# Kernel optimization log

Measured on AMD Instinct MI355X. Metric: run time of the kernel, lower is better.

## Reference

```python
import jax, jax.numpy as jnp
import numpy as np

DILATIONS = [1, 2, 4, 8, 16, 32, 64, 128, 256, 512] * 2  # 20 layers
C = 128      # residual channels
S = 128      # skip channels
K = 3        # kernel size
B = 8        # batch
T = 8192     # timesteps


def _causal_dilated_conv(x, W, b, dilation):
    # x: [B, Cin, T], W: [Cout, Cin, K] -> [B, Cout, T], left-padded (causal)
    pad = (W.shape[-1] - 1) * dilation
    y = jax.lax.conv_general_dilated(
        x, W, window_strides=(1,), padding=[(pad, 0)],
        rhs_dilation=(dilation,), dimension_numbers=('NCH', 'OIH', 'NCH'))
    return y + b[None, :, None]


def setup_inputs() -> dict:
    key = jax.random.key(0)
    ks = jax.random.split(key, 7)
    L = len(DILATIONS)
    scale = 0.05
    x = jax.random.normal(ks[0], (B, C, T), dtype=jnp.float32)
    # gated activation: dilated conv emits 2*C channels (tanh half + sigmoid half)
    Wconv = jax.random.normal(ks[1], (L, 2 * C, C, K), dtype=jnp.float32) * scale
    bconv = jax.random.normal(ks[2], (L, 2 * C), dtype=jnp.float32) * scale
    Wout = jax.random.normal(ks[3], (L, C, C), dtype=jnp.float32) * scale
    bout = jax.random.normal(ks[4], (L, C), dtype=jnp.float32) * scale
    Wskip = jax.random.normal(ks[5], (L, S, C), dtype=jnp.float32) * scale
    bskip = jax.random.normal(ks[6], (L, S), dtype=jnp.float32) * scale
    return {"x": x, "Wconv": Wconv, "bconv": bconv, "Wout": Wout,
            "bout": bout, "Wskip": Wskip, "bskip": bskip}


def reference(x, Wconv, bconv, Wout, bout, Wskip, bskip):
    L = len(DILATIONS)
    skips = []
    for i, d in enumerate(DILATIONS):
        y = _causal_dilated_conv(x, Wconv[i], bconv[i], d)       # [B, 2C, T]
        a, g = jnp.split(y, 2, axis=1)
        z = jnp.tanh(a) * jax.nn.sigmoid(g)                       # gated, [B, C, T]
        skips.append(jnp.einsum('sc,bct->bst', Wskip[i], z) + bskip[i][None, :, None])
        if i < L - 1:
            out = jnp.einsum('oc,bct->bot', Wout[i], z) + bout[i][None, :, None]
        else:
            out = z  # last layer: use_output_transform = False
        x = out + x  # residual add
    return x, jnp.stack(skips)  # ([B,C,T], [L,B,S,T])
```

## Files before the change

kernel.cpp:

```cpp
#include <hip/hip_runtime.h>
#include <hip/hip_bf16.h>

#define L_NUM 20
#define CC 128
#define TB 8192
#define BB 8
#define TT 64

#define NCONV (L_NUM * 3 * 256 * 128)
#define NMAT  (L_NUM * 128 * 128)
#define XN    ((size_t)BB * TB * CC)

typedef __attribute__((ext_vector_type(4))) float f32x4;
typedef __attribute__((ext_vector_type(8))) short bf16x8;
typedef unsigned int u32;

static const int DILS[L_NUM] = {1, 2, 4, 8, 16, 32, 64, 128, 256, 512,
                                1, 2, 4, 8, 16, 32, 64, 128, 256, 512};

__device__ __forceinline__ unsigned short f2b(float f) {
  union { __hip_bfloat16 h; unsigned short u; } cv;
  cv.h = __float2bfloat16(f);
  return cv.u;
}
__device__ __forceinline__ float b2fu(u32 u) {
  union { u32 u; float f; } cv;
  cv.u = u << 16;
  return cv.f;
}

__device__ __forceinline__ int swz(int t, int cbyte) {
  return (t * 256 + cbyte) ^ ((t & 7) << 4);
}

__device__ __forceinline__ void gload16(const void* g, void* l) {
  __builtin_amdgcn_global_load_lds(
      (const __attribute__((address_space(1))) u32*)g,
      (__attribute__((address_space(3))) u32*)l, 16, 0, 0);
}

__global__ void prep_kernel(const float* __restrict__ Wconv,
                            const float* __restrict__ Wout,
                            const float* __restrict__ Wskip,
                            unsigned short* __restrict__ wc,
                            unsigned short* __restrict__ wo,
                            unsigned short* __restrict__ wsk,
                            unsigned short* __restrict__ zp) {
  int i = blockIdx.x * 256 + threadIdx.x;
  if (i < 128) zp[i] = 0;
  if (i < NCONV) {
    int c = i & 127;
    int o = (i >> 7) & 255;
    int lk = i >> 15;
    int k = lk % 3;
    int l = lk / 3;
    wc[i] = f2b(Wconv[((size_t)(l * 256 + o) * 128 + c) * 3 + k]);
  }
  if (i < NMAT) {
    wo[i]  = f2b(Wout[i]);
    wsk[i] = f2b(Wskip[i]);
  }
}

__global__ __launch_bounds__(256) void x0t_kernel(const float* __restrict__ x0,
                                                  unsigned short* __restrict__ hi,
                                                  unsigned short* __restrict__ lo) {
  __shared__ unsigned short Hs[TT * CC], Ls[TT * CC];
  const int tid = threadIdx.x, lane = tid & 63, w = tid >> 6;
  const int b = blockIdx.y, t0 = blockIdx.x * TT;
  const float* xb = x0 + (size_t)b * CC * TB;
#pragma unroll
  for (int it = 0; it < 8; ++it) {
    int c0 = it * 16 + w * 4;
    u32 hu[4], lu[4];
#pragma unroll
    for (int i2 = 0; i2 < 4; ++i2) {
      float v = xb[(size_t)(c0 + i2) * TB + t0 + lane];
      unsigned short h = f2b(v);
      hu[i2] = h;
      lu[i2] = f2b(v - b2fu(h));
    }
    uint2 hp, lp;
    hp.x = hu[0] | (hu[1] << 16); hp.y = hu[2] | (hu[3] << 16);
    lp.x = lu[0] | (lu[1] << 16); lp.y = lu[2] | (lu[3] << 16);
    *reinterpret_cast<uint2*>(reinterpret_cast<char*>(Hs) + swz(lane, c0 * 2)) = hp;
    *reinterpret_cast<uint2*>(reinterpret_cast<char*>(Ls) + swz(lane, c0 * 2)) = lp;
  }
  __syncthreads();
  unsigned short* hb = hi + ((size_t)b * TB + t0) * CC;
  unsigned short* lb = lo + ((size_t)b * TB + t0) * CC;
#pragma unroll
  for (int it = 0; it < 4; ++it) {
    int o = it * 4096 + tid * 16;
    int t = o >> 8;
    int cl = o & 255;
    int li = t * 256 + (cl ^ ((t & 7) << 4));
    *reinterpret_cast<f32x4*>(reinterpret_cast<char*>(hb) + (size_t)t * 256 + cl) =
        *reinterpret_cast<f32x4*>(reinterpret_cast<char*>(Hs) + li);
    *reinterpret_cast<f32x4*>(reinterpret_cast<char*>(lb) + (size_t)t * 256 + cl) =
        *reinterpret_cast<f32x4*>(reinterpret_cast<char*>(Ls) + li);
  }
}

__global__ __launch_bounds__(512, 4) void layer_kernel(
    const unsigned short* __restrict__ hin,
    unsigned short* __restrict__ hout,
    unsigned short* __restrict__ lob,
    const unsigned short* __restrict__ zpage,
    const unsigned short* __restrict__ Wc,
    const float* __restrict__ bconv,
    const unsigned short* __restrict__ Wo,
    const float* __restrict__ bout,
    const unsigned short* __restrict__ Wsk,
    const float* __restrict__ bskip,
    float* __restrict__ skipo,
    float* __restrict__ fxout,
    int dil, int last) {
  __shared__ unsigned short Xs[3][TT * CC];
  unsigned short* Zs = &Xs[0][0];

  const int tid = threadIdx.x;
  const int lane = tid & 63;
  const int w = tid >> 6;
  const int lo16 = lane & 15;
  const int hi4 = lane >> 4;

  int p = blockIdx.x + (blockIdx.y << 7);
  int xcd = p & 7, ii = p >> 3;
  int bx = (xcd << 4) | (ii >> 3);
  int b = ii & 7;
  int t0 = bx * TT;

  const unsigned short* hb = hin + (size_t)b * TB * CC;

#pragma unroll
  for (int k = 0; k < 3; ++k) {
    int tbase = t0 + (k - 2) * dil;
#pragma unroll
    for (int i = 0; i < 2; ++i) {
      int o = w * 2048 + i * 1024 + lane * 16;
      int tl = o >> 8;
      int cb = (o & 255) ^ ((tl & 7) << 4);
      int tg = tbase + tl;
      const char* src = (tg >= 0)
          ? (reinterpret_cast<const char*>(hb + (size_t)tg * CC) + cb)
          : (reinterpret_cast<const char*>(zpage) + cb);
      gload16(src, reinterpret_cast<char*>(&Xs[k][0]) + w * 2048 + i * 1024);
    }
  }
  __syncthreads();

  f32x4 zero4 = {0.f, 0.f, 0.f, 0.f};
  f32x4 accA[4], accG[4];
#pragma unroll
  for (int j = 0; j < 4; ++j) { accA[j] = zero4; accG[j] = zero4; }

#pragma unroll
  for (int k = 0; k < 3; ++k) {
    const unsigned short* Wk = Wc + k * 256 * 128;
#pragma unroll
    for (int kk = 0; kk < 4; ++kk) {
      int c0 = kk * 32 + hi4 * 8;
      bf16x8 aA = *reinterpret_cast<const bf16x8*>(Wk + (w * 16 + lo16) * 128 + c0);
      bf16x8 aG = *reinterpret_cast<const bf16x8*>(Wk + (128 + w * 16 + lo16) * 128 + c0);
#pragma unroll
      for (int j = 0; j < 4; ++j) {
        bf16x8 bx8 = *reinterpret_cast<const bf16x8*>(
            reinterpret_cast<const char*>(&Xs[k][0]) + swz(j * 16 + lo16, c0 * 2));
        accA[j] = __builtin_amdgcn_mfma_f32_16x16x32_bf16(aA, bx8, accA[j], 0, 0, 0);
        accG[j] = __builtin_amdgcn_mfma_f32_16x16x32_bf16(aG, bx8, accG[j], 0, 0, 0);
      }
    }
  }

  f32x4 bca = *reinterpret_cast<const f32x4*>(bconv + w * 16 + hi4 * 4);
  f32x4 bcg = *reinterpret_cast<const f32x4*>(bconv + 128 + w * 16 + hi4 * 4);
  uint2 zpk[4];
#pragma unroll
  for (int j = 0; j < 4; ++j) {
    u32 zu[4];
#pragma unroll
    for (int reg = 0; reg < 4; ++reg) {
      float a = accA[j][reg] + bca[reg];
      float g = accG[j][reg] + bcg[reg];
      float ea = __builtin_amdgcn_exp2f(2.885390081777927f * a);
      float th = 1.f - 2.f * __builtin_amdgcn_rcpf(1.f + ea);
      float sg = __builtin_amdgcn_rcpf(
          1.f + __builtin_amdgcn_exp2f(-1.4426950408889634f * g));
      zu[reg] = f2b(th * sg);
    }
    zpk[j].x = zu[0] | (zu[1] << 16);
    zpk[j].y = zu[2] | (zu[3] << 16);
  }

  const unsigned short* lb = lob + (size_t)b * TB * CC;
  uint2 hres[4], lres[4];
#pragma unroll
  for (int j = 0; j < 4; ++j) {
    int t = t0 + j * 16 + lo16;
    int cB = w * 16 + hi4 * 4;
    hres[j] = *reinterpret_cast<const uint2*>(hb + (size_t)t * CC + cB);
    lres[j] = *reinterpret_cast<const uint2*>(lb + (size_t)t * CC + cB);
  }
  f32x4 bsk = *reinterpret_cast<const f32x4*>(bskip + w * 16 + hi4 * 4);
  f32x4 bo  = *reinterpret_cast<const f32x4*>(bout + w * 16 + hi4 * 4);

  __syncthreads();

#pragma unroll
  for (int j = 0; j < 4; ++j) {
    int cB = w * 16 + hi4 * 4;
    *reinterpret_cast<uint2*>(reinterpret_cast<char*>(Zs) +
                              swz(j * 16 + lo16, cB * 2)) = zpk[j];
  }
  __syncthreads();

  f32x4 accS[4], accO[4];
#pragma unroll
  for (int j = 0; j < 4; ++j) { accS[j] = zero4; accO[j] = zero4; }

#pragma unroll
  for (int kk = 0; kk < 4; ++kk) {
    int c0 = kk * 32 + hi4 * 8;
    bf16x8 aS = *reinterpret_cast<const bf16x8*>(Wsk + (w * 16 + lo16) * 128 + c0);
    bf16x8 aO = *reinterpret_cast<const bf16x8*>(Wo + (w * 16 + lo16) * 128 + c0);
#pragma unroll
    for (int j = 0; j < 4; ++j) {
      bf16x8 bz = *reinterpret_cast<const bf16x8*>(
          reinterpret_cast<const char*>(Zs) + swz(j * 16 + lo16, c0 * 2));
      accS[j] = __builtin_amdgcn_mfma_f32_16x16x32_bf16(aS, bz, accS[j], 0, 0, 0);
      accO[j] = __builtin_amdgcn_mfma_f32_16x16x32_bf16(aO, bz, accO[j], 0, 0, 0);
    }
  }

  float* skb = skipo + (size_t)b * CC * TB;
  float* fxb = fxout + (size_t)b * CC * TB;
  unsigned short* hrow = hout + (size_t)b * TB * CC;
  unsigned short* lrow = lob + (size_t)b * TB * CC;

#pragma unroll
  for (int j = 0; j < 4; ++j) {
    int t = j * 16 + lo16;
    int cB = w * 16 + hi4 * 4;
    u32 hu[4] = {hres[j].x & 0xffffu, hres[j].x >> 16,
                 hres[j].y & 0xffffu, hres[j].y >> 16};
    u32 lu[4] = {lres[j].x & 0xffffu, lres[j].x >> 16,
                 lres[j].y & 0xffffu, lres[j].y >> 16};
#pragma unroll
    for (int reg = 0; reg < 4; ++reg)
      skb[(size_t)(cB + reg) * TB + t0 + t] = accS[j][reg] + bsk[reg];
    if (last) {
      uint2 zp2 = *reinterpret_cast<const uint2*>(
          reinterpret_cast<const char*>(Zs) + swz(t, cB * 2));
      u32 zu[4] = {zp2.x & 0xffffu, zp2.x >> 16, zp2.y & 0xffffu, zp2.y >> 16};
#pragma unroll
      for (int reg = 0; reg < 4; ++reg)
        fxb[(size_t)(cB + reg) * TB + t0 + t] =
            b2fu(zu[reg]) + b2fu(hu[reg]) + b2fu(lu[reg]);
    } else {
      u32 ho[4], lo4[4];
#pragma unroll
      for (int reg = 0; reg < 4; ++reg) {
        float v = accO[j][reg] + bo[reg] + b2fu(hu[reg]) + b2fu(lu[reg]);
        unsigned short h = f2b(v);
        ho[reg] = h;
        lo4[reg] = f2b(v - b2fu(h));
      }
      uint2 hq, lq;
      hq.x = ho[0] | (ho[1] << 16); hq.y = ho[2] | (ho[3] << 16);
      lq.x = lo4[0] | (lo4[1] << 16); lq.y = lo4[2] | (lo4[3] << 16);
      *reinterpret_cast<uint2*>(hrow + (size_t)(t0 + t) * CC + cB) = hq;
      *reinterpret_cast<uint2*>(lrow + (size_t)(t0 + t) * CC + cB) = lq;
    }
  }
}

extern "C" void kernel_launch(void* const* d_in, const int* in_sizes, int n_in,
                              void* d_out, int out_size, void* d_ws, size_t ws_size,
                              hipStream_t stream) {
  const float* x0    = (const float*)d_in[0];
  const float* Wconv = (const float*)d_in[1];
  const float* bconv = (const float*)d_in[2];
  const float* Wout  = (const float*)d_in[3];
  const float* bout  = (const float*)d_in[4];
  const float* Wskip = (const float*)d_in[5];
  const float* bskip = (const float*)d_in[6];

  unsigned short* wc  = (unsigned short*)d_ws;
  unsigned short* wo  = wc + NCONV;
  unsigned short* wsk = wo + NMAT;
  unsigned short* zp  = wsk + NMAT;
  unsigned short* hiA = zp + 128;
  unsigned short* lob = hiA + XN;

  float* fx = (float*)d_out;
  float* skips = fx + XN;
  unsigned short* hiB = (unsigned short*)d_out;

  prep_kernel<<<(NCONV + 255) / 256, 256, 0, stream>>>(Wconv, Wout, Wskip, wc, wo, wsk, zp);
  x0t_kernel<<<dim3(TB / TT, BB), 256, 0, stream>>>(x0, hiB, lob);

  for (int l = 0; l < L_NUM; ++l) {
    const unsigned short* hin = (l % 2 == 0) ? hiB : hiA;
    unsigned short* hout      = (l % 2 == 0) ? hiA : hiB;
    layer_kernel<<<dim3(TB / TT, BB), 512, 0, stream>>>(
        hin, hout, lob, zp,
        wc + (size_t)l * 3 * 256 * 128, bconv + (size_t)l * 256,
        wo + (size_t)l * 128 * 128, bout + (size_t)l * 128,
        wsk + (size_t)l * 128 * 128, bskip + (size_t)l * 128,
        skips + (size_t)l * XN, fx,
        DILS[l], l == L_NUM - 1 ? 1 : 0);
  }
}
```

Baseline: 1.075 ms.

## Fuse all layers into one persistent cooperative kernel with double-buffered staging

Replaces the 20 per-layer launches with one cooperative persistent kernel of 256 blocks, each owning 256 timesteps of one batch item. Layers are separated by grid-wide syncs. Within a block, the next 64-step tile is prefetched into a second LDS buffer while the current one is computed. The low-precision residual part now stays in registers across layers instead of round-tripping through global memory, and the residual high part is read from the already staged LDS tile. This removes launch overhead and global traffic, at the cost of grid-sync latency, only 256 blocks (lower occupancy), and twice the LDS use.

```diff
diff --git a/kernel.cpp b/kernel.cpp
--- a/kernel.cpp
+++ b/kernel.cpp
@@ -1,5 +1,8 @@
 #include <hip/hip_runtime.h>
 #include <hip/hip_bf16.h>
+#include <hip/hip_cooperative_groups.h>
+
+namespace cg = cooperative_groups;
 
 #define L_NUM 20
 #define CC 128
@@ -15,8 +18,7 @@
 typedef __attribute__((ext_vector_type(8))) short bf16x8;
 typedef unsigned int u32;
 
-static const int DILS[L_NUM] = {1, 2, 4, 8, 16, 32, 64, 128, 256, 512,
-                                1, 2, 4, 8, 16, 32, 64, 128, 256, 512};
+#define MFMA16 __builtin_amdgcn_mfma_f32_16x16x32_bf16
 
 __device__ __forceinline__ unsigned short f2b(float f) {
   union { __hip_bfloat16 h; unsigned short u; } cv;
@@ -102,175 +104,205 @@
   }
 }
 
-__global__ __launch_bounds__(512, 4) void layer_kernel(
-    const unsigned short* __restrict__ hin,
-    unsigned short* __restrict__ hout,
-    unsigned short* __restrict__ lob,
+__global__ __launch_bounds__(512, 2) void stack_kernel(
+    unsigned short* __restrict__ hA,
+    unsigned short* __restrict__ hB,
+    const unsigned short* __restrict__ lo0,
     const unsigned short* __restrict__ zpage,
-    const unsigned short* __restrict__ Wc,
-    const float* __restrict__ bconv,
-    const unsigned short* __restrict__ Wo,
-    const float* __restrict__ bout,
-    const unsigned short* __restrict__ Wsk,
-    const float* __restrict__ bskip,
-    float* __restrict__ skipo,
-    float* __restrict__ fxout,
-    int dil, int last) {
-  __shared__ unsigned short Xs[3][TT * CC];
-  unsigned short* Zs = &Xs[0][0];
+    const unsigned short* __restrict__ wc,
+    const float* __restrict__ bconv_a,
+    const unsigned short* __restrict__ wo,
+    const float* __restrict__ bout_a,
+    const unsigned short* __restrict__ wsk,
+    const float* __restrict__ bskip_a,
+    float* __restrict__ skips,
+    float* __restrict__ fx) {
+  __shared__ unsigned short Xs[2][3][TT * CC];
 
   const int tid = threadIdx.x;
   const int lane = tid & 63;
   const int w = tid >> 6;
   const int lo16 = lane & 15;
   const int hi4 = lane >> 4;
-
-  int p = blockIdx.x + (blockIdx.y << 7);
-  int xcd = p & 7, ii = p >> 3;
-  int bx = (xcd << 4) | (ii >> 3);
-  int b = ii & 7;
-  int t0 = bx * TT;
-
-  const unsigned short* hb = hin + (size_t)b * TB * CC;
-
-#pragma unroll
-  for (int k = 0; k < 3; ++k) {
-    int tbase = t0 + (k - 2) * dil;
-#pragma unroll
-    for (int i = 0; i < 2; ++i) {
-      int o = w * 2048 + i * 1024 + lane * 16;
-      int tl = o >> 8;
-      int cb = (o & 255) ^ ((tl & 7) << 4);
-      int tg = tbase + tl;
-      const char* src = (tg >= 0)
-          ? (reinterpret_cast<const char*>(hb + (size_t)tg * CC) + cb)
-          : (reinterpret_cast<const char*>(zpage) + cb);
-      gload16(src, reinterpret_cast<char*>(&Xs[k][0]) + w * 2048 + i * 1024);
+  const int cB = w * 16 + hi4 * 4;
+
+  const int bid = blockIdx.x;
+  const int b = (bid >> 3) >> 2;
+  const int st0 = (bid & 7) * 1024 + ((bid >> 3) & 3) * 256;
+
+  uint2 lres[4][4];
+#pragma unroll
+  for (int i = 0; i < 4; ++i)
+#pragma unroll
+    for (int j = 0; j < 4; ++j)
+      lres[i][j] = *reinterpret_cast<const uint2*>(
+          lo0 + ((size_t)b * TB + st0 + i * 64 + j * 16 + lo16) * CC + cB);
+
+  auto STAGE = [&](const unsigned short* hbp, int t0_, int bufsel, int dil_) {
+#pragma unroll
+    for (int k = 0; k < 3; ++k) {
+      int tbase = t0_ + (k - 2) * dil_;
+#pragma unroll
+      for (int ii = 0; ii < 2; ++ii) {
+        int o = w * 2048 + ii * 1024 + lane * 16;
+        int tl = o >> 8;
+        int cb = (o & 255) ^ ((tl & 7) << 4);
+        int tg = tbase + tl;
+        const char* src = (tg >= 0)
+            ? (reinterpret_cast<const char*>(hbp + (size_t)tg * CC) + cb)
+            : (reinterpret_cast<const char*>(zpage) + cb);
+        gload16(src,
+                reinterpret_cast<char*>(&Xs[bufsel][k][0]) + w * 2048 + ii * 1024);
+      }
     }
-  }
-  __syncthreads();
-
-  f32x4 zero4 = {0.f, 0.f, 0.f, 0.f};
-  f32x4 accA[4], accG[4];
-#pragma unroll
-  for (int j = 0; j < 4; ++j) { accA[j] = zero4; accG[j] = zero4; }
-
-#pragma unroll
-  for (int k = 0; k < 3; ++k) {
-    const unsigned short* Wk = Wc + k * 256 * 128;
-#pragma unroll
-    for (int kk = 0; kk < 4; ++kk) {
-      int c0 = kk * 32 + hi4 * 8;
-      bf16x8 aA = *reinterpret_cast<const bf16x8*>(Wk + (w * 16 + lo16) * 128 + c0);
-      bf16x8 aG = *reinterpret_cast<const bf16x8*>(Wk + (128 + w * 16 + lo16) * 128 + c0);
+  };
+
+  STAGE(hB + (size_t)b * TB * CC, st0, 0, 1);
+
+  for (int l = 0; l < L_NUM; ++l) {
+    const int dil = 1 << (l % 10);
+    const unsigned short* hb = ((l & 1) ? hA : hB) + (size_t)b * TB * CC;
+    unsigned short* ho = ((l & 1) ? hB : hA) + (size_t)b * TB * CC;
+    const int last = (l == L_NUM - 1);
+    const unsigned short* Wc_l = wc + (size_t)l * 3 * 256 * 128;
+    const unsigned short* Wo_l = wo + (size_t)l * 128 * 128;
+    const unsigned short* Ws_l = wsk + (size_t)l * 128 * 128;
+    float* skb = skips + (size_t)l * XN + (size_t)b * CC * TB;
+    float* fxb = fx + (size_t)b * CC * TB;
+
+    f32x4 bca = *reinterpret_cast<const f32x4*>(bconv_a + l * 256 + cB);
+    f32x4 bcg = *reinterpret_cast<const f32x4*>(bconv_a + l * 256 + 128 + cB);
+    f32x4 bsk = *reinterpret_cast<const f32x4*>(bskip_a + l * 128 + cB);
+    f32x4 bo  = *reinterpret_cast<const f32x4*>(bout_a + l * 128 + cB);
+
+#pragma unroll
+    for (int i = 0; i < 4; ++i) {
+      const int cur = i & 1;
+      const int t0 = st0 + i * 64;
+
+      asm volatile("s_waitcnt vmcnt(0)" ::: "memory");
+      __builtin_amdgcn_s_barrier();
+      __builtin_amdgcn_sched_barrier(0);
+      asm volatile("" ::: "memory");
+
+      if (i < 3) STAGE(hb, st0 + (i + 1) * 64, cur ^ 1, dil);
+
+      f32x4 zero4 = {0.f, 0.f, 0.f, 0.f};
+      f32x4 accA[4], accG[4];
+#pragma unroll
+      for (int j = 0; j < 4; ++j) { accA[j] = zero4; accG[j] = zero4; }
+
+#pragma unroll
+      for (int k = 0; k < 3; ++k) {
+        const unsigned short* Wk = Wc_l + k * 256 * 128;
+#pragma unroll
+        for (int kk = 0; kk < 4; ++kk) {
+          int c0 = kk * 32 + hi4 * 8;
+          bf16x8 aA = *reinterpret_cast<const bf16x8*>(Wk + (w * 16 + lo16) * 128 + c0);
+          bf16x8 aG = *reinterpret_cast<const bf16x8*>(Wk + (128 + w * 16 + lo16) * 128 + c0);
+#pragma unroll
+          for (int j = 0; j < 4; ++j) {
+            bf16x8 bx8 = *reinterpret_cast<const bf16x8*>(
+                reinterpret_cast<const char*>(&Xs[cur][k][0]) + swz(j * 16 + lo16, c0 * 2));
+            accA[j] = MFMA16(aA, bx8, accA[j], 0, 0, 0);
+            accG[j] = MFMA16(aG, bx8, accG[j], 0, 0, 0);
+          }
+        }
+      }
+
+      uint2 zpk[4];
 #pragma unroll
       for (int j = 0; j < 4; ++j) {
-        bf16x8 bx8 = *reinterpret_cast<const bf16x8*>(
-            reinterpret_cast<const char*>(&Xs[k][0]) + swz(j * 16 + lo16, c0 * 2));
-        accA[j] = __builtin_amdgcn_mfma_f32_16x16x32_bf16(aA, bx8, accA[j], 0, 0, 0);
-        accG[j] = __builtin_amdgcn_mfma_f32_16x16x32_bf16(aG, bx8, accG[j], 0, 0, 0);
+        u32 zu[4];
+#pragma unroll
+        for (int reg = 0; reg < 4; ++reg) {
+          float a = accA[j][reg] + bca[reg];
+          float g = accG[j][reg] + bcg[reg];
+          float ea = __builtin_amdgcn_exp2f(2.885390081777927f * a);
+          float th = 1.f - 2.f * __builtin_amdgcn_rcpf(1.f + ea);
+          float sg = __builtin_amdgcn_rcpf(
+              1.f + __builtin_amdgcn_exp2f(-1.4426950408889634f * g));
+          zu[reg] = f2b(th * sg);
+        }
+        zpk[j].x = zu[0] | (zu[1] << 16);
+        zpk[j].y = zu[2] | (zu[3] << 16);
+      }
+
+      asm volatile("" ::: "memory");
+      __builtin_amdgcn_s_barrier();
+      __builtin_amdgcn_sched_barrier(0);
+      asm volatile("" ::: "memory");
+
+#pragma unroll
+      for (int j = 0; j < 4; ++j)
+        *reinterpret_cast<uint2*>(reinterpret_cast<char*>(&Xs[cur][0][0]) +
+                                  swz(j * 16 + lo16, cB * 2)) = zpk[j];
+
+      asm volatile("s_waitcnt lgkmcnt(0)" ::: "memory");
+      __builtin_amdgcn_s_barrier();
+      __builtin_amdgcn_sched_barrier(0);
+      asm volatile("" ::: "memory");
+
+      f32x4 accS[4], accO[4];
+#pragma unroll
+      for (int j = 0; j < 4; ++j) { accS[j] = zero4; accO[j] = zero4; }
+
+#pragma unroll
+      for (int kk = 0; kk < 4; ++kk) {
+        int c0 = kk * 32 + hi4 * 8;
+        bf16x8 aS = *reinterpret_cast<const bf16x8*>(Ws_l + (w * 16 + lo16) * 128 + c0);
+        bf16x8 aO = *reinterpret_cast<const bf16x8*>(Wo_l + (w * 16 + lo16) * 128 + c0);
+#pragma unroll
+        for (int j = 0; j < 4; ++j) {
+          bf16x8 bz = *reinterpret_cast<const bf16x8*>(
+              reinterpret_cast<const char*>(&Xs[cur][0][0]) + swz(j * 16 + lo16, c0 * 2));
+          accS[j] = MFMA16(aS, bz, accS[j], 0, 0, 0);
+          accO[j] = MFMA16(aO, bz, accO[j], 0, 0, 0);
+        }
+      }
+
+#pragma unroll
+      for (int j = 0; j < 4; ++j) {
+        int t = j * 16 + lo16;
+        uint2 hp = *reinterpret_cast<const uint2*>(
+            reinterpret_cast<const char*>(&Xs[cur][2][0]) + swz(t, cB * 2));
+        u32 hu[4] = {hp.x & 0xffffu, hp.x >> 16, hp.y & 0xffffu, hp.y >> 16};
+        u32 lu[4] = {lres[i][j].x & 0xffffu, lres[i][j].x >> 16,
+                     lres[i][j].y & 0xffffu, lres[i][j].y >> 16};
+#pragma unroll
+        for (int reg = 0; reg < 4; ++reg)
+          skb[(size_t)(cB + reg) * TB + t0 + t] = accS[j][reg] + bsk[reg];
+        if (last) {
+          uint2 zp2 = *reinterpret_cast<const uint2*>(
+              reinterpret_cast<const char*>(&Xs[cur][0][0]) + swz(t, cB * 2));
+          u32 zu[4] = {zp2.x & 0xffffu, zp2.x >> 16, zp2.y & 0xffffu, zp2.y >> 16};
+#pragma unroll
+          for (int reg = 0; reg < 4; ++reg)
+            fxb[(size_t)(cB + reg) * TB + t0 + t] =
+                b2fu(zu[reg]) + b2fu(hu[reg]) + b2fu(lu[reg]);
+        } else {
+          u32 hn[4], ln[4];
+#pragma unroll
+          for (int reg = 0; reg < 4; ++reg) {
+            float v = accO[j][reg] + bo[reg] + b2fu(hu[reg]) + b2fu(lu[reg]);
+            unsigned short h = f2b(v);
+            hn[reg] = h;
+            ln[reg] = f2b(v - b2fu(h));
+          }
+          uint2 hq;
+          hq.x = hn[0] | (hn[1] << 16); hq.y = hn[2] | (hn[3] << 16);
+          *reinterpret_cast<uint2*>(ho + (size_t)(t0 + t) * CC + cB) = hq;
+          lres[i][j].x = ln[0] | (ln[1] << 16);
+          lres[i][j].y = ln[2] | (ln[3] << 16);
+        }
       }
     }
-  }
-
-  f32x4 bca = *reinterpret_cast<const f32x4*>(bconv + w * 16 + hi4 * 4);
-  f32x4 bcg = *reinterpret_cast<const f32x4*>(bconv + 128 + w * 16 + hi4 * 4);
-  uint2 zpk[4];
-#pragma unroll
-  for (int j = 0; j < 4; ++j) {
-    u32 zu[4];
-#pragma unroll
-    for (int reg = 0; reg < 4; ++reg) {
-      float a = accA[j][reg] + bca[reg];
-      float g = accG[j][reg] + bcg[reg];
-      float ea = __builtin_amdgcn_exp2f(2.885390081777927f * a);
-      float th = 1.f - 2.f * __builtin_amdgcn_rcpf(1.f + ea);
-      float sg = __builtin_amdgcn_rcpf(
-          1.f + __builtin_amdgcn_exp2f(-1.4426950408889634f * g));
-      zu[reg] = f2b(th * sg);
-    }
-    zpk[j].x = zu[0] | (zu[1] << 16);
-    zpk[j].y = zu[2] | (zu[3] << 16);
-  }
-
-  const unsigned short* lb = lob + (size_t)b * TB * CC;
-  uint2 hres[4], lres[4];
-#pragma unroll
-  for (int j = 0; j < 4; ++j) {
-    int t = t0 + j * 16 + lo16;
-    int cB = w * 16 + hi4 * 4;
-    hres[j] = *reinterpret_cast<const uint2*>(hb + (size_t)t * CC + cB);
-    lres[j] = *reinterpret_cast<const uint2*>(lb + (size_t)t * CC + cB);
-  }
-  f32x4 bsk = *reinterpret_cast<const f32x4*>(bskip + w * 16 + hi4 * 4);
-  f32x4 bo  = *reinterpret_cast<const f32x4*>(bout + w * 16 + hi4 * 4);
-
-  __syncthreads();
-
-#pragma unroll
-  for (int j = 0; j < 4; ++j) {
-    int cB = w * 16 + hi4 * 4;
-    *reinterpret_cast<uint2*>(reinterpret_cast<char*>(Zs) +
-                              swz(j * 16 + lo16, cB * 2)) = zpk[j];
-  }
-  __syncthreads();
-
-  f32x4 accS[4], accO[4];
-#pragma unroll
-  for (int j = 0; j < 4; ++j) { accS[j] = zero4; accO[j] = zero4; }
-
-#pragma unroll
-  for (int kk = 0; kk < 4; ++kk) {
-    int c0 = kk * 32 + hi4 * 8;
-    bf16x8 aS = *reinterpret_cast<const bf16x8*>(Wsk + (w * 16 + lo16) * 128 + c0);
-    bf16x8 aO = *reinterpret_cast<const bf16x8*>(Wo + (w * 16 + lo16) * 128 + c0);
-#pragma unroll
-    for (int j = 0; j < 4; ++j) {
-      bf16x8 bz = *reinterpret_cast<const bf16x8*>(
-          reinterpret_cast<const char*>(Zs) + swz(j * 16 + lo16, c0 * 2));
-      accS[j] = __builtin_amdgcn_mfma_f32_16x16x32_bf16(aS, bz, accS[j], 0, 0, 0);
-      accO[j] = __builtin_amdgcn_mfma_f32_16x16x32_bf16(aO, bz, accO[j], 0, 0, 0);
-    }
-  }
-
-  float* skb = skipo + (size_t)b * CC * TB;
-  float* fxb = fxout + (size_t)b * CC * TB;
-  unsigned short* hrow = hout + (size_t)b * TB * CC;
-  unsigned short* lrow = lob + (size_t)b * TB * CC;
-
-#pragma unroll
-  for (int j = 0; j < 4; ++j) {
-    int t = j * 16 + lo16;
-    int cB = w * 16 + hi4 * 4;
-    u32 hu[4] = {hres[j].x & 0xffffu, hres[j].x >> 16,
-                 hres[j].y & 0xffffu, hres[j].y >> 16};
-    u32 lu[4] = {lres[j].x & 0xffffu, lres[j].x >> 16,
-                 lres[j].y & 0xffffu, lres[j].y >> 16};
-#pragma unroll
-    for (int reg = 0; reg < 4; ++reg)
-      skb[(size_t)(cB + reg) * TB + t0 + t] = accS[j][reg] + bsk[reg];
-    if (last) {
-      uint2 zp2 = *reinterpret_cast<const uint2*>(
-          reinterpret_cast<const char*>(Zs) + swz(t, cB * 2));
-      u32 zu[4] = {zp2.x & 0xffffu, zp2.x >> 16, zp2.y & 0xffffu, zp2.y >> 16};
-#pragma unroll
-      for (int reg = 0; reg < 4; ++reg)
-        fxb[(size_t)(cB + reg) * TB + t0 + t] =
-            b2fu(zu[reg]) + b2fu(hu[reg]) + b2fu(lu[reg]);
-    } else {
-      u32 ho[4], lo4[4];
-#pragma unroll
-      for (int reg = 0; reg < 4; ++reg) {
-        float v = accO[j][reg] + bo[reg] + b2fu(hu[reg]) + b2fu(lu[reg]);
-        unsigned short h = f2b(v);
-        ho[reg] = h;
-        lo4[reg] = f2b(v - b2fu(h));
-      }
-      uint2 hq, lq;
-      hq.x = ho[0] | (ho[1] << 16); hq.y = ho[2] | (ho[3] << 16);
-      lq.x = lo4[0] | (lo4[1] << 16); lq.y = lo4[2] | (lo4[3] << 16);
-      *reinterpret_cast<uint2*>(hrow + (size_t)(t0 + t) * CC + cB) = hq;
-      *reinterpret_cast<uint2*>(lrow + (size_t)(t0 + t) * CC + cB) = lq;
+
+    if (!last) {
+      __threadfence();
+      cg::this_grid().sync();
+      const unsigned short* hbn = (((l + 1) & 1) ? hA : hB) + (size_t)b * TB * CC;
+      STAGE(hbn, st0, 0, 1 << ((l + 1) % 10));
     }
   }
 }
@@ -290,25 +322,19 @@
   unsigned short* wo  = wc + NCONV;
   unsigned short* wsk = wo + NMAT;
   unsigned short* zp  = wsk + NMAT;
-  unsigned short* hiA = zp + 128;
-  unsigned short* lob = hiA + XN;
+  unsigned short* hA  = zp + 128;
+  unsigned short* lo  = hA + XN;
 
   float* fx = (float*)d_out;
   float* skips = fx + XN;
-  unsigned short* hiB = (unsigned short*)d_out;
+  unsigned short* hB = (unsigned short*)d_out;
 
   prep_kernel<<<(NCONV + 255) / 256, 256, 0, stream>>>(Wconv, Wout, Wskip, wc, wo, wsk, zp);
-  x0t_kernel<<<dim3(TB / TT, BB), 256, 0, stream>>>(x0, hiB, lob);
-
-  for (int l = 0; l < L_NUM; ++l) {
-    const unsigned short* hin = (l % 2 == 0) ? hiB : hiA;
-    unsigned short* hout      = (l % 2 == 0) ? hiA : hiB;
-    layer_kernel<<<dim3(TB / TT, BB), 512, 0, stream>>>(
-        hin, hout, lob, zp,
-        wc + (size_t)l * 3 * 256 * 128, bconv + (size_t)l * 256,
-        wo + (size_t)l * 128 * 128, bout + (size_t)l * 128,
-        wsk + (size_t)l * 128 * 128, bskip + (size_t)l * 128,
-        skips + (size_t)l * XN, fx,
-        DILS[l], l == L_NUM - 1 ? 1 : 0);
-  }
-}
+  x0t_kernel<<<dim3(TB / TT, BB), 256, 0, stream>>>(x0, hB, lo);
+
+  void* args[] = {(void*)&hA, (void*)&hB, (void*)&lo, (void*)&zp,
+                  (void*)&wc, (void*)&bconv, (void*)&wo, (void*)&bout,
+                  (void*)&wsk, (void*)&bskip, (void*)&skips, (void*)&fx};
+  hipLaunchCooperativeKernel((const void*)stack_kernel, dim3(256), dim3(512),
+                             args, 0, stream);
+}
```

Result: slower. 3.132 ms (+191.3%).

## Halve time tile, use 4-wave blocks with 32 channels per wave, reuse LDS residual

Applied to the files above, without the earlier changes.

The layer kernel now uses 32-timestep tiles and 256-thread blocks. Each wave computes 32 output channels, so every loaded weight fragment feeds more MFMAs, and the grid doubles with a new block-to-XCD mapping. The high half of the residual is read from the already-staged k=2 LDS tile instead of being reloaded from global memory, and the low half is prefetched before the first barrier. Skip and final outputs use nontemporal stores. Risks are extra register pressure from twice as many accumulators and more redundant halo/weight loads per timestep with the smaller tile.

```diff
diff --git a/kernel.cpp b/kernel.cpp
--- a/kernel.cpp
+++ b/kernel.cpp
@@ -5,7 +5,7 @@
 #define CC 128
 #define TB 8192
 #define BB 8
-#define TT 64
+#define TT 32
 
 #define NCONV (L_NUM * 3 * 256 * 128)
 #define NMAT  (L_NUM * 128 * 128)
@@ -14,6 +14,8 @@
 typedef __attribute__((ext_vector_type(4))) float f32x4;
 typedef __attribute__((ext_vector_type(8))) short bf16x8;
 typedef unsigned int u32;
+
+#define MFMA16 __builtin_amdgcn_mfma_f32_16x16x32_bf16
 
 static const int DILS[L_NUM] = {1, 2, 4, 8, 16, 32, 64, 128, 256, 512,
                                 1, 2, 4, 8, 16, 32, 64, 128, 256, 512};
@@ -65,9 +67,9 @@
 __global__ __launch_bounds__(256) void x0t_kernel(const float* __restrict__ x0,
                                                   unsigned short* __restrict__ hi,
                                                   unsigned short* __restrict__ lo) {
-  __shared__ unsigned short Hs[TT * CC], Ls[TT * CC];
+  __shared__ unsigned short Hs[64 * CC], Ls[64 * CC];
   const int tid = threadIdx.x, lane = tid & 63, w = tid >> 6;
-  const int b = blockIdx.y, t0 = blockIdx.x * TT;
+  const int b = blockIdx.y, t0 = blockIdx.x * 64;
   const float* xb = x0 + (size_t)b * CC * TB;
 #pragma unroll
   for (int it = 0; it < 8; ++it) {
@@ -102,7 +104,7 @@
   }
 }
 
-__global__ __launch_bounds__(512, 4) void layer_kernel(
+__global__ __launch_bounds__(256, 5) void layer_kernel(
     const unsigned short* __restrict__ hin,
     unsigned short* __restrict__ hout,
     unsigned short* __restrict__ lob,
@@ -125,11 +127,10 @@
   const int lo16 = lane & 15;
   const int hi4 = lane >> 4;
 
-  int p = blockIdx.x + (blockIdx.y << 7);
+  int p = blockIdx.x;
   int xcd = p & 7, ii = p >> 3;
-  int bx = (xcd << 4) | (ii >> 3);
-  int b = ii & 7;
-  int t0 = bx * TT;
+  int t0 = (xcd * 32 + ii) * TT;
+  int b = blockIdx.y;
 
   const unsigned short* hb = hin + (size_t)b * TB * CC;
 
@@ -138,22 +139,34 @@
     int tbase = t0 + (k - 2) * dil;
 #pragma unroll
     for (int i = 0; i < 2; ++i) {
-      int o = w * 2048 + i * 1024 + lane * 16;
+      int o = (w * 2 + i) * 1024 + lane * 16;
       int tl = o >> 8;
       int cb = (o & 255) ^ ((tl & 7) << 4);
       int tg = tbase + tl;
       const char* src = (tg >= 0)
           ? (reinterpret_cast<const char*>(hb + (size_t)tg * CC) + cb)
           : (reinterpret_cast<const char*>(zpage) + cb);
-      gload16(src, reinterpret_cast<char*>(&Xs[k][0]) + w * 2048 + i * 1024);
-    }
-  }
+      gload16(src, reinterpret_cast<char*>(&Xs[k][0]) + (w * 2 + i) * 1024);
+    }
+  }
+
+  const unsigned short* lb = lob + (size_t)b * TB * CC;
+  uint2 lres[2][2];
+#pragma unroll
+  for (int r = 0; r < 2; ++r)
+#pragma unroll
+    for (int j = 0; j < 2; ++j)
+      lres[r][j] = *reinterpret_cast<const uint2*>(
+          lb + (size_t)(t0 + j * 16 + lo16) * CC + w * 32 + r * 16 + hi4 * 4);
+
   __syncthreads();
 
   f32x4 zero4 = {0.f, 0.f, 0.f, 0.f};
-  f32x4 accA[4], accG[4];
-#pragma unroll
-  for (int j = 0; j < 4; ++j) { accA[j] = zero4; accG[j] = zero4; }
+  f32x4 accA[2][2], accG[2][2];
+#pragma unroll
+  for (int r = 0; r < 2; ++r)
+#pragma unroll
+    for (int j = 0; j < 2; ++j) { accA[r][j] = zero4; accG[r][j] = zero4; }
 
 #pragma unroll
   for (int k = 0; k < 3; ++k) {
@@ -161,75 +174,76 @@
 #pragma unroll
     for (int kk = 0; kk < 4; ++kk) {
       int c0 = kk * 32 + hi4 * 8;
-      bf16x8 aA = *reinterpret_cast<const bf16x8*>(Wk + (w * 16 + lo16) * 128 + c0);
-      bf16x8 aG = *reinterpret_cast<const bf16x8*>(Wk + (128 + w * 16 + lo16) * 128 + c0);
-#pragma unroll
-      for (int j = 0; j < 4; ++j) {
+      bf16x8 aA0 = *reinterpret_cast<const bf16x8*>(Wk + (w * 32 + lo16) * 128 + c0);
+      bf16x8 aA1 = *reinterpret_cast<const bf16x8*>(Wk + (w * 32 + 16 + lo16) * 128 + c0);
+      bf16x8 aG0 = *reinterpret_cast<const bf16x8*>(Wk + (128 + w * 32 + lo16) * 128 + c0);
+      bf16x8 aG1 = *reinterpret_cast<const bf16x8*>(Wk + (128 + w * 32 + 16 + lo16) * 128 + c0);
+#pragma unroll
+      for (int j = 0; j < 2; ++j) {
         bf16x8 bx8 = *reinterpret_cast<const bf16x8*>(
             reinterpret_cast<const char*>(&Xs[k][0]) + swz(j * 16 + lo16, c0 * 2));
-        accA[j] = __builtin_amdgcn_mfma_f32_16x16x32_bf16(aA, bx8, accA[j], 0, 0, 0);
-        accG[j] = __builtin_amdgcn_mfma_f32_16x16x32_bf16(aG, bx8, accG[j], 0, 0, 0);
+        accA[0][j] = MFMA16(aA0, bx8, accA[0][j], 0, 0, 0);
+        accA[1][j] = MFMA16(aA1, bx8, accA[1][j], 0, 0, 0);
+        accG[0][j] = MFMA16(aG0, bx8, accG[0][j], 0, 0, 0);
+        accG[1][j] = MFMA16(aG1, bx8, accG[1][j], 0, 0, 0);
       }
     }
   }
 
-  f32x4 bca = *reinterpret_cast<const f32x4*>(bconv + w * 16 + hi4 * 4);
-  f32x4 bcg = *reinterpret_cast<const f32x4*>(bconv + 128 + w * 16 + hi4 * 4);
-  uint2 zpk[4];
-#pragma unroll
-  for (int j = 0; j < 4; ++j) {
-    u32 zu[4];
-#pragma unroll
-    for (int reg = 0; reg < 4; ++reg) {
-      float a = accA[j][reg] + bca[reg];
-      float g = accG[j][reg] + bcg[reg];
-      float ea = __builtin_amdgcn_exp2f(2.885390081777927f * a);
-      float th = 1.f - 2.f * __builtin_amdgcn_rcpf(1.f + ea);
-      float sg = __builtin_amdgcn_rcpf(
-          1.f + __builtin_amdgcn_exp2f(-1.4426950408889634f * g));
-      zu[reg] = f2b(th * sg);
-    }
-    zpk[j].x = zu[0] | (zu[1] << 16);
-    zpk[j].y = zu[2] | (zu[3] << 16);
-  }
-
-  const unsigned short* lb = lob + (size_t)b * TB * CC;
-  uint2 hres[4], lres[4];
-#pragma unroll
-  for (int j = 0; j < 4; ++j) {
-    int t = t0 + j * 16 + lo16;
-    int cB = w * 16 + hi4 * 4;
-    hres[j] = *reinterpret_cast<const uint2*>(hb + (size_t)t * CC + cB);
-    lres[j] = *reinterpret_cast<const uint2*>(lb + (size_t)t * CC + cB);
-  }
-  f32x4 bsk = *reinterpret_cast<const f32x4*>(bskip + w * 16 + hi4 * 4);
-  f32x4 bo  = *reinterpret_cast<const f32x4*>(bout + w * 16 + hi4 * 4);
+  uint2 zpk[2][2];
+#pragma unroll
+  for (int r = 0; r < 2; ++r) {
+    f32x4 bca = *reinterpret_cast<const f32x4*>(bconv + w * 32 + r * 16 + hi4 * 4);
+    f32x4 bcg = *reinterpret_cast<const f32x4*>(bconv + 128 + w * 32 + r * 16 + hi4 * 4);
+#pragma unroll
+    for (int j = 0; j < 2; ++j) {
+      u32 zu[4];
+#pragma unroll
+      for (int reg = 0; reg < 4; ++reg) {
+        float a = accA[r][j][reg] + bca[reg];
+        float g = accG[r][j][reg] + bcg[reg];
+        float ea = __builtin_amdgcn_exp2f(2.885390081777927f * a);
+        float th = 1.f - 2.f * __builtin_amdgcn_rcpf(1.f + ea);
+        float sg = __builtin_amdgcn_rcpf(
+            1.f + __builtin_amdgcn_exp2f(-1.4426950408889634f * g));
+        zu[reg] = f2b(th * sg);
+      }
+      zpk[r][j].x = zu[0] | (zu[1] << 16);
+      zpk[r][j].y = zu[2] | (zu[3] << 16);
+    }
+  }
 
   __syncthreads();
 
 #pragma unroll
-  for (int j = 0; j < 4; ++j) {
-    int cB = w * 16 + hi4 * 4;
-    *reinterpret_cast<uint2*>(reinterpret_cast<char*>(Zs) +
-                              swz(j * 16 + lo16, cB * 2)) = zpk[j];
-  }
+  for (int r = 0; r < 2; ++r)
+#pragma unroll
+    for (int j = 0; j < 2; ++j)
+      *reinterpret_cast<uint2*>(reinterpret_cast<char*>(Zs) +
+          swz(j * 16 + lo16, (w * 32 + r * 16 + hi4 * 4) * 2)) = zpk[r][j];
   __syncthreads();
 
-  f32x4 accS[4], accO[4];
-#pragma unroll
-  for (int j = 0; j < 4; ++j) { accS[j] = zero4; accO[j] = zero4; }
+  f32x4 accS[2][2], accO[2][2];
+#pragma unroll
+  for (int r = 0; r < 2; ++r)
+#pragma unroll
+    for (int j = 0; j < 2; ++j) { accS[r][j] = zero4; accO[r][j] = zero4; }
 
 #pragma unroll
   for (int kk = 0; kk < 4; ++kk) {
     int c0 = kk * 32 + hi4 * 8;
-    bf16x8 aS = *reinterpret_cast<const bf16x8*>(Wsk + (w * 16 + lo16) * 128 + c0);
-    bf16x8 aO = *reinterpret_cast<const bf16x8*>(Wo + (w * 16 + lo16) * 128 + c0);
-#pragma unroll
-    for (int j = 0; j < 4; ++j) {
+    bf16x8 aS0 = *reinterpret_cast<const bf16x8*>(Wsk + (w * 32 + lo16) * 128 + c0);
+    bf16x8 aS1 = *reinterpret_cast<const bf16x8*>(Wsk + (w * 32 + 16 + lo16) * 128 + c0);
+    bf16x8 aO0 = *reinterpret_cast<const bf16x8*>(Wo + (w * 32 + lo16) * 128 + c0);
+    bf16x8 aO1 = *reinterpret_cast<const bf16x8*>(Wo + (w * 32 + 16 + lo16) * 128 + c0);
+#pragma unroll
+    for (int j = 0; j < 2; ++j) {
       bf16x8 bz = *reinterpret_cast<const bf16x8*>(
           reinterpret_cast<const char*>(Zs) + swz(j * 16 + lo16, c0 * 2));
-      accS[j] = __builtin_amdgcn_mfma_f32_16x16x32_bf16(aS, bz, accS[j], 0, 0, 0);
-      accO[j] = __builtin_amdgcn_mfma_f32_16x16x32_bf16(aO, bz, accO[j], 0, 0, 0);
+      accS[0][j] = MFMA16(aS0, bz, accS[0][j], 0, 0, 0);
+      accS[1][j] = MFMA16(aS1, bz, accS[1][j], 0, 0, 0);
+      accO[0][j] = MFMA16(aO0, bz, accO[0][j], 0, 0, 0);
+      accO[1][j] = MFMA16(aO1, bz, accO[1][j], 0, 0, 0);
     }
   }
 
@@ -239,38 +253,45 @@
   unsigned short* lrow = lob + (size_t)b * TB * CC;
 
 #pragma unroll
-  for (int j = 0; j < 4; ++j) {
-    int t = j * 16 + lo16;
-    int cB = w * 16 + hi4 * 4;
-    u32 hu[4] = {hres[j].x & 0xffffu, hres[j].x >> 16,
-                 hres[j].y & 0xffffu, hres[j].y >> 16};
-    u32 lu[4] = {lres[j].x & 0xffffu, lres[j].x >> 16,
-                 lres[j].y & 0xffffu, lres[j].y >> 16};
-#pragma unroll
-    for (int reg = 0; reg < 4; ++reg)
-      skb[(size_t)(cB + reg) * TB + t0 + t] = accS[j][reg] + bsk[reg];
-    if (last) {
-      uint2 zp2 = *reinterpret_cast<const uint2*>(
-          reinterpret_cast<const char*>(Zs) + swz(t, cB * 2));
-      u32 zu[4] = {zp2.x & 0xffffu, zp2.x >> 16, zp2.y & 0xffffu, zp2.y >> 16};
+  for (int r = 0; r < 2; ++r) {
+    f32x4 bsk = *reinterpret_cast<const f32x4*>(bskip + w * 32 + r * 16 + hi4 * 4);
+    f32x4 bo  = *reinterpret_cast<const f32x4*>(bout + w * 32 + r * 16 + hi4 * 4);
+#pragma unroll
+    for (int j = 0; j < 2; ++j) {
+      int t = j * 16 + lo16;
+      int cB = w * 32 + r * 16 + hi4 * 4;
+      uint2 hp = *reinterpret_cast<const uint2*>(
+          reinterpret_cast<const char*>(&Xs[2][0]) + swz(t, cB * 2));
+      u32 hu[4] = {hp.x & 0xffffu, hp.x >> 16, hp.y & 0xffffu, hp.y >> 16};
+      u32 lu[4] = {lres[r][j].x & 0xffffu, lres[r][j].x >> 16,
+                   lres[r][j].y & 0xffffu, lres[r][j].y >> 16};
 #pragma unroll
       for (int reg = 0; reg < 4; ++reg)
-        fxb[(size_t)(cB + reg) * TB + t0 + t] =
-            b2fu(zu[reg]) + b2fu(hu[reg]) + b2fu(lu[reg]);
-    } else {
-      u32 ho[4], lo4[4];
-#pragma unroll
-      for (int reg = 0; reg < 4; ++reg) {
-        float v = accO[j][reg] + bo[reg] + b2fu(hu[reg]) + b2fu(lu[reg]);
-        unsigned short h = f2b(v);
-        ho[reg] = h;
-        lo4[reg] = f2b(v - b2fu(h));
+        __builtin_nontemporal_store(accS[r][j][reg] + bsk[reg],
+                                    skb + (size_t)(cB + reg) * TB + t0 + t);
+      if (last) {
+        uint2 zp2 = *reinterpret_cast<const uint2*>(
+            reinterpret_cast<const char*>(Zs) + swz(t, cB * 2));
+        u32 zu[4] = {zp2.x & 0xffffu, zp2.x >> 16, zp2.y & 0xffffu, zp2.y >> 16};
+#pragma unroll
+        for (int reg = 0; reg < 4; ++reg)
+          __builtin_nontemporal_store(b2fu(zu[reg]) + b2fu(hu[reg]) + b2fu(lu[reg]),
+                                      fxb + (size_t)(cB + reg) * TB + t0 + t);
+      } else {
+        u32 hn[4], ln[4];
+#pragma unroll
+        for (int reg = 0; reg < 4; ++reg) {
+          float v = accO[r][j][reg] + bo[reg] + b2fu(hu[reg]) + b2fu(lu[reg]);
+          unsigned short h = f2b(v);
+          hn[reg] = h;
+          ln[reg] = f2b(v - b2fu(h));
+        }
+        uint2 hq, lq;
+        hq.x = hn[0] | (hn[1] << 16); hq.y = hn[2] | (hn[3] << 16);
+        lq.x = ln[0] | (ln[1] << 16); lq.y = ln[2] | (ln[3] << 16);
+        *reinterpret_cast<uint2*>(hrow + (size_t)(t0 + t) * CC + cB) = hq;
+        *reinterpret_cast<uint2*>(lrow + (size_t)(t0 + t) * CC + cB) = lq;
       }
-      uint2 hq, lq;
-      hq.x = ho[0] | (ho[1] << 16); hq.y = ho[2] | (ho[3] << 16);
-      lq.x = lo4[0] | (lo4[1] << 16); lq.y = lo4[2] | (lo4[3] << 16);
-      *reinterpret_cast<uint2*>(hrow + (size_t)(t0 + t) * CC + cB) = hq;
-      *reinterpret_cast<uint2*>(lrow + (size_t)(t0 + t) * CC + cB) = lq;
     }
   }
 }
@@ -298,12 +319,12 @@
   unsigned short* hiB = (unsigned short*)d_out;
 
   prep_kernel<<<(NCONV + 255) / 256, 256, 0, stream>>>(Wconv, Wout, Wskip, wc, wo, wsk, zp);
-  x0t_kernel<<<dim3(TB / TT, BB), 256, 0, stream>>>(x0, hiB, lob);
+  x0t_kernel<<<dim3(TB / 64, BB), 256, 0, stream>>>(x0, hiB, lob);
 
   for (int l = 0; l < L_NUM; ++l) {
     const unsigned short* hin = (l % 2 == 0) ? hiB : hiA;
     unsigned short* hout      = (l % 2 == 0) ? hiA : hiB;
-    layer_kernel<<<dim3(TB / TT, BB), 512, 0, stream>>>(
+    layer_kernel<<<dim3(TB / TT, BB), 256, 0, stream>>>(
         hin, hout, lob, zp,
         wc + (size_t)l * 3 * 256 * 128, bconv + (size_t)l * 256,
         wo + (size_t)l * 128 * 128, bout + (size_t)l * 128,
```

New measurement: 1.537 ms. 42.9% more time.
